# Kernel tuning notes

Hardware: AMD Instinct MI355X
Metric: run time of the kernel (lower is better)

Reference implementation:

```python
import jax, jax.numpy as jnp
import numpy as np

N, F_IN, HID, C, H = 4096, 1024, 64, 40, 8
ALPHA = 0.2  # LeakyReLU negative slope
NEG_INF = -9e15

def setup_inputs() -> dict:
    key = jax.random.key(0)
    ks = jax.random.split(key, 8)
    x = jax.random.normal(ks[0], (N, F_IN), jnp.float32)
    adj = jax.random.randint(ks[1], (N, N), 0, 2, jnp.int32)  # dense 0/1 adjacency
    W = jax.random.normal(ks[2], (H, F_IN, HID), jnp.float32) / np.sqrt(F_IN).astype(np.float32)
    a_src = jax.random.normal(ks[3], (H, HID), jnp.float32) * 0.1
    a_dst = jax.random.normal(ks[4], (H, HID), jnp.float32) * 0.1
    W_out = jax.random.normal(ks[5], (H * HID, C), jnp.float32) / np.sqrt(H * HID).astype(np.float32)
    ao_src = jax.random.normal(ks[6], (C,), jnp.float32) * 0.1
    ao_dst = jax.random.normal(ks[7], (C,), jnp.float32) * 0.1
    return dict(x=x, adj=adj, W=W, a_src=a_src, a_dst=a_dst,
                W_out=W_out, ao_src=ao_src, ao_dst=ao_dst)

def _masked_attention(src, dst, mask):
    # src: [..., N] scores for row node i; dst: [..., N] scores for col node j
    e = jax.nn.leaky_relu(src[..., :, None] + dst[..., None, :], ALPHA)  # [..., N, N]
    e = jnp.where(mask, e, NEG_INF)
    return jax.nn.softmax(e, axis=-1)

def reference(x, adj, W, a_src, a_dst, W_out, ao_src, ao_dst):
    mask = adj > 0  # [N, N]
    # multi-head GAT layer (concat=True)
    Wh = jnp.einsum('nf,hfo->hno', x, W)            # [H, N, HID]
    src = jnp.einsum('hno,ho->hn', Wh, a_src)       # [H, N]
    dst = jnp.einsum('hno,ho->hn', Wh, a_dst)       # [H, N]
    att = _masked_attention(src, dst, mask[None])   # [H, N, N]
    h = jnp.einsum('hij,hjo->hio', att, Wh)         # [H, N, HID]
    h = jax.nn.elu(h)                               # concat=True -> elu inside layer
    h = jnp.transpose(h, (1, 0, 2)).reshape(N, H * HID)  # concat heads -> [N, H*HID]
    # output GAT layer (concat=False -> no elu inside)
    Wh2 = h @ W_out                                 # [N, C]
    att2 = _masked_attention(Wh2 @ ao_src, Wh2 @ ao_dst, mask)  # [N, N]
    out = att2 @ Wh2                                # [N, C]
    # model-level: elu then log_softmax over classes
    return jax.nn.log_softmax(jax.nn.elu(out), axis=1)
```

## Files before the change

kernel.cpp:

```cpp
#include <hip/hip_runtime.h>

#define NN 4096
#define F_IN 1024
#define NHEAD 8
#define HID 64
#define NCLS 40
#define LOG2E 1.44269504f

typedef float f32x4 __attribute__((ext_vector_type(4)));
typedef float f32x2 __attribute__((ext_vector_type(2)));
typedef short s16x8 __attribute__((ext_vector_type(8)));

#define SWZ(r,c) (((r)*64) + ((c) ^ (((r)&7)<<3)))

__device__ __forceinline__ unsigned short f2bf(float f){
  unsigned u = __float_as_uint(f);
  return (unsigned short)((u + 0x7fffu + ((u >> 16) & 1u)) >> 16);
}
__device__ __forceinline__ float bf2f(unsigned short u){
  return __uint_as_float((unsigned)u << 16);
}
__device__ __forceinline__ unsigned cvtpk(float lo, float hi){
  unsigned r; asm("v_cvt_pk_bf16_f32 %0, %1, %2" : "=v"(r) : "v"(lo), "v"(hi)); return r;
}
__device__ __forceinline__ f32x2 pkmul(f32x2 a, f32x2 b){
  f32x2 r; asm("v_pk_mul_f32 %0, %1, %2" : "=v"(r) : "v"(a), "v"(b)); return r;
}

__global__ __launch_bounds__(256) void pack_adj_k(const int* __restrict__ adj, unsigned* __restrict__ bmT){
  int gid = blockIdx.x*256 + threadIdx.x;
  int lane = threadIdx.x & 63;
  unsigned long long m = __ballot(adj[gid] > 0);
  int w = gid >> 5, i = w >> 7, jw = w & 127;
  if (lane == 0)       bmT[(size_t)jw*NN + i] = (unsigned)m;
  else if (lane == 32) bmT[(size_t)jw*NN + i] = (unsigned)(m >> 32);
}

__global__ __launch_bounds__(256) void cast_W_k(const float* __restrict__ W, unsigned short* __restrict__ WbT){
  __shared__ float T[64][65];
  const int h = blockIdx.y, k0 = blockIdx.x*64, t = threadIdx.x;
  for (int idx = t; idx < 1024; idx += 256){
    int k = idx >> 4, c4 = idx & 15;
    *(float4*)&T[k][c4*4] = *(const float4*)&W[((size_t)h*F_IN + k0 + k)*HID + c4*4];
  }
  __syncthreads();
  for (int idx = t; idx < 512; idx += 256){
    int o = idx >> 3, ch = idx & 7;
    s16x8 v;
    #pragma unroll
    for (int e = 0; e < 8; ++e) v[e] = (short)f2bf(T[ch*8 + e][o]);
    *(s16x8*)&WbT[((size_t)h*HID + o)*F_IN + k0 + ch*8] = v;
  }
}

__global__ __launch_bounds__(256) void cast_Wo_k(const float* __restrict__ Wout, unsigned short* __restrict__ WoT){
  int idx = blockIdx.x*256 + threadIdx.x;
  int cc = idx >> 9, k = idx & 511;
  WoT[idx] = (cc < NCLS) ? f2bf(Wout[(size_t)k*NCLS + cc]) : (unsigned short)0;
}

__global__ __launch_bounds__(256) void gemm1_k(const float* __restrict__ x,
    const unsigned short* __restrict__ WbT, unsigned short* __restrict__ WhT,
    const float* __restrict__ a_src, const float* __restrict__ a_dst,
    float* __restrict__ srcv, float* __restrict__ dstv, float2* __restrict__ bdv){
  __shared__ unsigned short xS[64*64];
  __shared__ unsigned short wS[64*64];
  const int t = threadIdx.x, l = t & 63, wv = t >> 6, g = l >> 4, c = l & 15;
  const int h = blockIdx.y, n0 = blockIdx.x * 64;
  f32x4 acc[4] = {};
  for (int k0 = 0; k0 < F_IN; k0 += 64){
    __syncthreads();
    #pragma unroll
    for (int p = 0; p < 4; ++p){
      int idx = t + p*256, row = idx >> 4, c4 = idx & 15;
      float4 v = *(const float4*)&x[(size_t)(n0+row)*F_IN + k0 + c4*4];
      *(uint2*)&xS[SWZ(row, c4*4)] = make_uint2(cvtpk(v.x, v.y), cvtpk(v.z, v.w));
    }
    #pragma unroll
    for (int p = 0; p < 2; ++p){
      int idx = t + p*256, o = idx >> 3, ch = idx & 7;
      *(s16x8*)&wS[SWZ(o, ch*8)] = *(const s16x8*)&WbT[(size_t)(h*HID + o)*F_IN + k0 + ch*8];
    }
    __syncthreads();
    #pragma unroll
    for (int ks = 0; ks < 2; ++ks){
      s16x8 av = *(const s16x8*)&xS[SWZ(wv*16 + c, ks*32 + g*8)];
      #pragma unroll
      for (int ct = 0; ct < 4; ++ct){
        s16x8 bv = *(const s16x8*)&wS[SWZ(ct*16 + c, ks*32 + g*8)];
        acc[ct] = __builtin_amdgcn_mfma_f32_16x16x32_bf16(av, bv, acc[ct], 0, 0, 0);
      }
    }
  }
  float asv[4], adv[4];
  #pragma unroll
  for (int ct = 0; ct < 4; ++ct){ asv[ct] = a_src[h*HID + ct*16 + c]; adv[ct] = a_dst[h*HID + ct*16 + c]; }
  #pragma unroll
  for (int r = 0; r < 4; ++r){
    float ps = acc[0][r]*asv[0] + acc[1][r]*asv[1] + acc[2][r]*asv[2] + acc[3][r]*asv[3];
    float pd = acc[0][r]*adv[0] + acc[1][r]*adv[1] + acc[2][r]*adv[2] + acc[3][r]*adv[3];
    #pragma unroll
    for (int off = 1; off < 16; off <<= 1){ ps += __shfl_xor(ps, off); pd += __shfl_xor(pd, off); }
    if (c == 0){
      int n = n0 + wv*16 + g*4 + r;
      srcv[h*NN + n] = ps; dstv[h*NN + n] = pd;
      bdv[h*NN + n] = make_float2(exp2f(pd*LOG2E), exp2f(0.2f*pd*LOG2E));
    }
  }
  __syncthreads();
  #pragma unroll
  for (int ct = 0; ct < 4; ++ct)
    *(uint2*)&xS[SWZ(ct*16 + c, wv*16 + g*4)] = make_uint2(cvtpk(acc[ct][0], acc[ct][1]), cvtpk(acc[ct][2], acc[ct][3]));
  __syncthreads();
  #pragma unroll
  for (int p = 0; p < 2; ++p){
    int idx = t + p*256, o = idx >> 3, ch = idx & 7;
    *(s16x8*)&WhT[(size_t)(h*HID + o)*NN + n0 + ch*8] = *(const s16x8*)&xS[SWZ(o, ch*8)];
  }
}

__global__ __launch_bounds__(256) void maxred_k(const float* __restrict__ in, float* __restrict__ out){
  __shared__ float red[4];
  const float* p = in + (size_t)blockIdx.x*NN;
  float m = -3.0e38f;
  for (int i = threadIdx.x; i < NN; i += 256) m = fmaxf(m, p[i]);
  #pragma unroll
  for (int off = 32; off; off >>= 1) m = fmaxf(m, __shfl_xor(m, off));
  if ((threadIdx.x & 63) == 0) red[threadIdx.x >> 6] = m;
  __syncthreads();
  if (threadIdx.x == 0) out[blockIdx.x] = fmaxf(fmaxf(red[0], red[1]), fmaxf(red[2], red[3]));
}

template<int NCT, int NJT, int MODE>
__global__ __launch_bounds__(256) void agg_mfma_k(
    const unsigned* __restrict__ bmT, const unsigned short* __restrict__ VT,
    const float* __restrict__ srcv, const float2* __restrict__ bdv,
    const float* __restrict__ maxp, void* __restrict__ partOut, float* __restrict__ denOut)
{
  __shared__ unsigned short vS[2][NCT*16*64];
  __shared__ float2 dS[2][64];
  __shared__ unsigned bitS[2][2][64];
  const int t = threadIdx.x, l = t & 63, wv = t >> 6, g = l >> 4, c = l & 15;
  const int h  = (MODE == 0) ? (blockIdx.y >> 2) : 0;
  const int ck = (MODE == 0) ? (blockIdx.y & 3)  : blockIdx.y;
  const int jt0 = ck * NJT;
  const int i0 = blockIdx.x * 64;
  const int lr = wv*16 + c;
  const float sr = srcv[h*NN + i0 + lr];
  const float mx = maxp[MODE == 0 ? h : 0];
  const float tm = sr + mx;
  const float mi2 = fmaxf(tm, 0.2f*tm) * LOG2E;
  f32x2 ac2;
  ac2[0] = exp2f(fmaf(sr, LOG2E, -mi2));
  ac2[1] = exp2f(fmaf(0.2f*sr, LOG2E, -mi2));
  const unsigned short* vb = VT + (MODE == 0 ? (size_t)h*HID*NN : (size_t)0);
  const float2* bp = bdv + (MODE == 0 ? (size_t)h*NN : (size_t)0);

  f32x4 acc[NCT] = {};
  f32x4 accs = {};
  s16x8 ones;
  #pragma unroll
  for (int e = 0; e < 8; ++e) ones[e] = (short)0x3F80;

  s16x8 vreg[2]; float2 dreg = make_float2(0.f, 0.f); unsigned breg = 0;
  auto loadRegs = [&](int jt){
    #pragma unroll
    for (int p = 0; p < 2; ++p){
      int u = t + p*256;
      if (u < NCT*128){
        int o = u >> 3, chk = u & 7;
        vreg[p] = *(const s16x8*)&vb[(size_t)o*NN + jt*64 + chk*8];
      }
    }
    if (t < 64) { f32x2 bd = *(const f32x2*)&bp[jt*64 + t]; dreg = make_float2(bd[0], bd[1]); }
    else if (t < 192){ int u = t - 64; breg = bmT[(size_t)(jt*2 + (u>>6))*NN + i0 + (u & 63)]; }
  };
  auto writeLDS = [&](int b){
    #pragma unroll
    for (int p = 0; p < 2; ++p){
      int u = t + p*256;
      if (u < NCT*128){
        int o = u >> 3, chk = u & 7;
        *(s16x8*)&vS[b][SWZ(o, chk*8)] = vreg[p];
      }
    }
    if (t < 64) dS[b][t] = dreg;
    else if (t < 192){ int u = t - 64; bitS[b][u>>6][u&63] = breg; }
  };
  auto computeBuf = [&](int b){
    #pragma unroll
    for (int ks = 0; ks < 2; ++ks){
      unsigned wb = (bitS[b][ks][lr] >> (g*8)) & 0xffu;
      const f32x2* dr = (const f32x2*)&dS[b][ks*32 + g*8];
      float q[8];
      #pragma unroll
      for (int e = 0; e < 8; ++e){
        f32x2 pr = pkmul(ac2, dr[e]);
        float m3 = __builtin_amdgcn_fmed3f(pr[0], pr[1], 1.0f);
        q[e] = (wb & (1u << e)) ? m3 : 0.f;
      }
      s16x8 afr;
      ((unsigned*)&afr)[0] = cvtpk(q[0], q[1]);
      ((unsigned*)&afr)[1] = cvtpk(q[2], q[3]);
      ((unsigned*)&afr)[2] = cvtpk(q[4], q[5]);
      ((unsigned*)&afr)[3] = cvtpk(q[6], q[7]);
      #pragma unroll
      for (int ct = 0; ct < NCT; ++ct){
        s16x8 bv = *(const s16x8*)&vS[b][SWZ(ct*16 + c, ks*32 + g*8)];
        acc[ct] = __builtin_amdgcn_mfma_f32_16x16x32_bf16(afr, bv, acc[ct], 0, 0, 0);
      }
      accs = __builtin_amdgcn_mfma_f32_16x16x32_bf16(afr, ones, accs, 0, 0, 0);
    }
  };

  loadRegs(jt0);
  writeLDS(0);
  __syncthreads();
  int cur = 0;
  for (int jj = 0; jj < NJT; ++jj){
    const bool more = (jj + 1 < NJT);
    if (more) loadRegs(jt0 + jj + 1);
    computeBuf(cur);
    if (more) writeLDS(cur ^ 1);
    __syncthreads();
    cur ^= 1;
  }

  if (MODE == 0){
    unsigned short* ob = (unsigned short*)partOut + (size_t)ck * NN * (NHEAD*HID);
    #pragma unroll
    for (int r = 0; r < 4; ++r){
      int row = i0 + wv*16 + g*4 + r;
      #pragma unroll
      for (int ct = 0; ct < NCT; ++ct)
        ob[(size_t)row*(NHEAD*HID) + h*HID + ct*16 + c] = f2bf(acc[ct][r]);
      if (c == 0) denOut[(size_t)(ck*NHEAD + h)*NN + row] = accs[r];
    }
  } else {
    float* ob = (float*)partOut + (size_t)ck * NN * 64;
    #pragma unroll
    for (int r = 0; r < 4; ++r){
      int row = i0 + wv*16 + g*4 + r;
      #pragma unroll
      for (int ct = 0; ct < NCT; ++ct)
        ob[(size_t)row*64 + ct*16 + c] = acc[ct][r];
      if (c == 0) ob[(size_t)row*64 + 48] = accs[r];
    }
  }
}

__global__ __launch_bounds__(256) void merge1_k(const unsigned short* __restrict__ part,
                                                const float* __restrict__ den,
                                                unsigned short* __restrict__ hb){
  int idx = blockIdx.x*256 + threadIdx.x;
  int row = idx >> 7, q = idx & 127;
  int h = q >> 4;
  float v[4] = {0.f, 0.f, 0.f, 0.f};
  float dn = 0.f;
  #pragma unroll
  for (int ck = 0; ck < 4; ++ck){
    const unsigned short* pb = part + ((size_t)ck*NN + row)*(NHEAD*HID) + q*4;
    ushort4 u = *(const ushort4*)pb;
    v[0] += bf2f(u.x); v[1] += bf2f(u.y); v[2] += bf2f(u.z); v[3] += bf2f(u.w);
    dn += den[(size_t)(ck*NHEAD + h)*NN + row];
  }
  float inv = 1.f / fmaxf(dn, 1e-30f);
  #pragma unroll
  for (int e = 0; e < 4; ++e){
    float x = v[e]*inv;
    v[e] = x > 0.f ? x : __expf(x) - 1.f;
  }
  *(uint2*)&hb[(size_t)row*(NHEAD*HID) + q*4] = make_uint2(cvtpk(v[0], v[1]), cvtpk(v[2], v[3]));
}

__global__ __launch_bounds__(256) void gemm2_k(const unsigned short* __restrict__ hb,
    const unsigned short* __restrict__ WoT, const float* __restrict__ aos, const float* __restrict__ aod,
    unsigned short* __restrict__ WhT2, float* __restrict__ s2, float* __restrict__ d2,
    float2* __restrict__ bd2){
  __shared__ unsigned short aS[64*64];
  __shared__ unsigned short bS[48*64];
  const int t = threadIdx.x, l = t & 63, wv = t >> 6, g = l >> 4, c = l & 15;
  const int n0 = blockIdx.x * 64;
  f32x4 acc[3] = {};
  for (int k0 = 0; k0 < NHEAD*HID; k0 += 64){
    __syncthreads();
    #pragma unroll
    for (int p = 0; p < 2; ++p){
      int u = t + p*256, o = u >> 3, ch = u & 7;
      *(s16x8*)&aS[SWZ(o, ch*8)] = *(const s16x8*)&hb[(size_t)(n0+o)*(NHEAD*HID) + k0 + ch*8];
    }
    for (int u = t; u < 384; u += 256){
      int o = u >> 3, ch = u & 7;
      *(s16x8*)&bS[SWZ(o, ch*8)] = *(const s16x8*)&WoT[(size_t)o*(NHEAD*HID) + k0 + ch*8];
    }
    __syncthreads();
    #pragma unroll
    for (int ks = 0; ks < 2; ++ks){
      s16x8 av = *(const s16x8*)&aS[SWZ(wv*16 + c, ks*32 + g*8)];
      #pragma unroll
      for (int ct = 0; ct < 3; ++ct){
        s16x8 bv = *(const s16x8*)&bS[SWZ(ct*16 + c, ks*32 + g*8)];
        acc[ct] = __builtin_amdgcn_mfma_f32_16x16x32_bf16(av, bv, acc[ct], 0, 0, 0);
      }
    }
  }
  float asv[3], adv[3];
  #pragma unroll
  for (int ct = 0; ct < 3; ++ct){
    int col = ct*16 + c;
    asv[ct] = (col < NCLS) ? aos[col] : 0.f;
    adv[ct] = (col < NCLS) ? aod[col] : 0.f;
  }
  #pragma unroll
  for (int r = 0; r < 4; ++r){
    float ps = acc[0][r]*asv[0] + acc[1][r]*asv[1] + acc[2][r]*asv[2];
    float pd = acc[0][r]*adv[0] + acc[1][r]*adv[1] + acc[2][r]*adv[2];
    #pragma unroll
    for (int off = 1; off < 16; off <<= 1){ ps += __shfl_xor(ps, off); pd += __shfl_xor(pd, off); }
    if (c == 0){
      int n = n0 + wv*16 + g*4 + r;
      s2[n] = ps; d2[n] = pd;
      bd2[n] = make_float2(exp2f(pd*LOG2E), exp2f(0.2f*pd*LOG2E));
    }
  }
  __syncthreads();
  #pragma unroll
  for (int ct = 0; ct < 3; ++ct)
    *(uint2*)&bS[SWZ(ct*16 + c, wv*16 + g*4)] = make_uint2(cvtpk(acc[ct][0], acc[ct][1]), cvtpk(acc[ct][2], acc[ct][3]));
  __syncthreads();
  for (int u = t; u < 384; u += 256){
    int o = u >> 3, ch = u & 7;
    *(s16x8*)&WhT2[(size_t)o*NN + n0 + ch*8] = *(const s16x8*)&bS[SWZ(o, ch*8)];
  }
}

__global__ __launch_bounds__(256) void final_k(const float* __restrict__ part, float* __restrict__ out){
  const int wid = (blockIdx.x*256 + threadIdx.x) >> 6;
  const int c = threadIdx.x & 63;
  float acc = 0.f, rs = 0.f;
  #pragma unroll
  for (int ch = 0; ch < 16; ++ch){
    const float* pb = part + ((size_t)ch*NN + wid)*64;
    if (c < 48) acc += pb[c];
    rs += pb[48];
  }
  float v = acc / fmaxf(rs, 1e-30f);
  float e = v > 0.f ? v : __expf(v) - 1.f;
  float ev = (c < NCLS) ? e : -3.0e38f;
  float m = ev;
  #pragma unroll
  for (int off = 32; off; off >>= 1) m = fmaxf(m, __shfl_xor(m, off));
  float ex = (c < NCLS) ? __expf(e - m) : 0.f;
  float s = ex;
  #pragma unroll
  for (int off = 32; off; off >>= 1) s += __shfl_xor(s, off);
  if (c < NCLS) out[(size_t)wid*NCLS + c] = e - m - __logf(s);
}

extern "C" void kernel_launch(void* const* d_in, const int* in_sizes, int n_in,
                              void* d_out, int out_size, void* d_ws, size_t ws_size,
                              hipStream_t stream){
  (void)in_sizes; (void)n_in; (void)out_size; (void)ws_size;
  const float* x     = (const float*)d_in[0];
  const int*   adj   = (const int*)  d_in[1];
  const float* W     = (const float*)d_in[2];
  const float* a_src = (const float*)d_in[3];
  const float* a_dst = (const float*)d_in[4];
  const float* W_out = (const float*)d_in[5];
  const float* aos   = (const float*)d_in[6];
  const float* aod   = (const float*)d_in[7];
  float* out = (float*)d_out;

  char* p = (char*)d_ws;
  unsigned* bmT        = (unsigned*)p;       p += (size_t)NN*128*4;
  unsigned short* WbT  = (unsigned short*)p; p += (size_t)NHEAD*HID*F_IN*2;
  unsigned short* WhT  = (unsigned short*)p; p += (size_t)NHEAD*HID*NN*2;
  unsigned short* hbuf = (unsigned short*)p; p += (size_t)NN*NHEAD*HID*2;
  unsigned short* WoT  = (unsigned short*)p; p += (size_t)48*NHEAD*HID*2;
  unsigned short* WhT2 = (unsigned short*)p; p += (size_t)48*NN*2;
  float* srcv = (float*)p; p += (size_t)NHEAD*NN*4;
  float* dstv = (float*)p; p += (size_t)NHEAD*NN*4;
  float* maxd = (float*)p; p += 256;
  float* s2   = (float*)p; p += (size_t)NN*4;
  float* d2   = (float*)p; p += (size_t)NN*4;
  float* m2   = (float*)p; p += 256;
  float2* bdv1 = (float2*)p; p += (size_t)NHEAD*NN*8;
  float2* bdv2 = (float2*)p; p += (size_t)NN*8;
  float* den1 = (float*)p; p += (size_t)4*NHEAD*NN*4;
  char* partU = p; p += (size_t)16*NN*64*4;

  pack_adj_k<<<(NN*NN)/256, 256, 0, stream>>>(adj, bmT);
  cast_W_k<<<dim3(F_IN/64, NHEAD), 256, 0, stream>>>(W, WbT);
  cast_Wo_k<<<96, 256, 0, stream>>>(W_out, WoT);
  gemm1_k<<<dim3(NN/64, NHEAD), 256, 0, stream>>>(x, WbT, WhT, a_src, a_dst, srcv, dstv, bdv1);
  maxred_k<<<NHEAD, 256, 0, stream>>>(dstv, maxd);
  agg_mfma_k<4, 16, 0><<<dim3(NN/64, NHEAD*4), 256, 0, stream>>>(bmT, WhT, srcv, bdv1, maxd, partU, den1);
  merge1_k<<<(NN*128)/256, 256, 0, stream>>>((const unsigned short*)partU, den1, hbuf);
  gemm2_k<<<NN/64, 256, 0, stream>>>(hbuf, WoT, aos, aod, WhT2, s2, d2, bdv2);
  maxred_k<<<1, 256, 0, stream>>>(d2, m2);
  agg_mfma_k<3, 4, 1><<<dim3(NN/64, 16), 256, 0, stream>>>(bmT, WhT2, s2, bdv2, m2, partU, nullptr);
  final_k<<<NN/4, 256, 0, stream>>>((const float*)partU, out);
}
```

Before: 160.4 us.

## Use 32x32 MFMA tiles for layer-1 attention aggregation with 8-way j split

Replaces the layer-1 aggregation kernel with a dedicated version using 32x32x16 bf16 MFMA over 128-row tiles, covering all 64 hidden columns per wave. The denominator is now summed in VALU from the probabilities rather than by an extra MFMA against a ones vector. The j range is split into 8 chunks instead of 4, and the merge kernel and workspace sizes are updated to match. This aims to raise MFMA efficiency and reuse of the value tile per row block, at the cost of more partial outputs to write and merge.

Result: no change. 159.1 us (-0.8%).

```diff
diff --git a/kernel.cpp b/kernel.cpp
--- a/kernel.cpp
+++ b/kernel.cpp
@@ -9,6 +9,7 @@
 
 typedef float f32x4 __attribute__((ext_vector_type(4)));
 typedef float f32x2 __attribute__((ext_vector_type(2)));
+typedef float f32x16 __attribute__((ext_vector_type(16)));
 typedef short s16x8 __attribute__((ext_vector_type(8)));
 
 #define SWZ(r,c) (((r)*64) + ((c) ^ (((r)&7)<<3)))
@@ -131,67 +132,59 @@
   if (threadIdx.x == 0) out[blockIdx.x] = fmaxf(fmaxf(red[0], red[1]), fmaxf(red[2], red[3]));
 }
 
-template<int NCT, int NJT, int MODE>
-__global__ __launch_bounds__(256) void agg_mfma_k(
+template<int NJT>
+__global__ __launch_bounds__(256) void agg32_k(
     const unsigned* __restrict__ bmT, const unsigned short* __restrict__ VT,
     const float* __restrict__ srcv, const float2* __restrict__ bdv,
-    const float* __restrict__ maxp, void* __restrict__ partOut, float* __restrict__ denOut)
+    const float* __restrict__ maxp, unsigned short* __restrict__ partOut, float* __restrict__ denOut)
 {
-  __shared__ unsigned short vS[2][NCT*16*64];
+  __shared__ unsigned short vS[2][64*64];
   __shared__ float2 dS[2][64];
-  __shared__ unsigned bitS[2][2][64];
-  const int t = threadIdx.x, l = t & 63, wv = t >> 6, g = l >> 4, c = l & 15;
-  const int h  = (MODE == 0) ? (blockIdx.y >> 2) : 0;
-  const int ck = (MODE == 0) ? (blockIdx.y & 3)  : blockIdx.y;
+  __shared__ unsigned bitS[2][2][128];
+  const int t = threadIdx.x, l = t & 63, wv = t >> 6, hk = l >> 5, lr31 = l & 31;
+  const int h  = blockIdx.y >> 3;
+  const int ck = blockIdx.y & 7;
   const int jt0 = ck * NJT;
-  const int i0 = blockIdx.x * 64;
-  const int lr = wv*16 + c;
+  const int i0 = blockIdx.x * 128;
+  const int lr = wv*32 + lr31;
   const float sr = srcv[h*NN + i0 + lr];
-  const float mx = maxp[MODE == 0 ? h : 0];
+  const float mx = maxp[h];
   const float tm = sr + mx;
   const float mi2 = fmaxf(tm, 0.2f*tm) * LOG2E;
   f32x2 ac2;
   ac2[0] = exp2f(fmaf(sr, LOG2E, -mi2));
   ac2[1] = exp2f(fmaf(0.2f*sr, LOG2E, -mi2));
-  const unsigned short* vb = VT + (MODE == 0 ? (size_t)h*HID*NN : (size_t)0);
-  const float2* bp = bdv + (MODE == 0 ? (size_t)h*NN : (size_t)0);
-
-  f32x4 acc[NCT] = {};
-  f32x4 accs = {};
-  s16x8 ones;
-  #pragma unroll
-  for (int e = 0; e < 8; ++e) ones[e] = (short)0x3F80;
+  const unsigned short* vb = VT + (size_t)h*HID*NN;
+  const float2* bp = bdv + (size_t)h*NN;
+
+  f32x16 acc[2] = {};
+  float rs = 0.f;
 
   s16x8 vreg[2]; float2 dreg = make_float2(0.f, 0.f); unsigned breg = 0;
   auto loadRegs = [&](int jt){
     #pragma unroll
     for (int p = 0; p < 2; ++p){
-      int u = t + p*256;
-      if (u < NCT*128){
-        int o = u >> 3, chk = u & 7;
-        vreg[p] = *(const s16x8*)&vb[(size_t)o*NN + jt*64 + chk*8];
-      }
-    }
-    if (t < 64) { f32x2 bd = *(const f32x2*)&bp[jt*64 + t]; dreg = make_float2(bd[0], bd[1]); }
-    else if (t < 192){ int u = t - 64; breg = bmT[(size_t)(jt*2 + (u>>6))*NN + i0 + (u & 63)]; }
+      int u = t + p*256, o = u >> 3, chk = u & 7;
+      vreg[p] = *(const s16x8*)&vb[(size_t)o*NN + jt*64 + chk*8];
+    }
+    if (t < 64){ f32x2 bd = *(const f32x2*)&bp[jt*64 + t]; dreg = make_float2(bd[0], bd[1]); }
+    breg = bmT[(size_t)(jt*2 + (t>>7))*NN + i0 + (t & 127)];
   };
   auto writeLDS = [&](int b){
     #pragma unroll
     for (int p = 0; p < 2; ++p){
-      int u = t + p*256;
-      if (u < NCT*128){
-        int o = u >> 3, chk = u & 7;
-        *(s16x8*)&vS[b][SWZ(o, chk*8)] = vreg[p];
-      }
+      int u = t + p*256, o = u >> 3, chk = u & 7;
+      *(s16x8*)&vS[b][SWZ(o, chk*8)] = vreg[p];
     }
     if (t < 64) dS[b][t] = dreg;
-    else if (t < 192){ int u = t - 64; bitS[b][u>>6][u&63] = breg; }
+    bitS[b][t>>7][t & 127] = breg;
   };
   auto computeBuf = [&](int b){
     #pragma unroll
-    for (int ks = 0; ks < 2; ++ks){
-      unsigned wb = (bitS[b][ks][lr] >> (g*8)) & 0xffu;
-      const f32x2* dr = (const f32x2*)&dS[b][ks*32 + g*8];
+    for (int ksl = 0; ksl < 4; ++ksl){
+      const int b0 = ksl*16 + hk*8;
+      unsigned wb = (bitS[b][b0 >> 5][lr] >> (b0 & 31)) & 0xffu;
+      const f32x2* dr = (const f32x2*)&dS[b][b0];
       float q[8];
       #pragma unroll
       for (int e = 0; e < 8; ++e){
@@ -199,17 +192,17 @@
         float m3 = __builtin_amdgcn_fmed3f(pr[0], pr[1], 1.0f);
         q[e] = (wb & (1u << e)) ? m3 : 0.f;
       }
+      rs += ((q[0]+q[1])+(q[2]+q[3])) + ((q[4]+q[5])+(q[6]+q[7]));
       s16x8 afr;
       ((unsigned*)&afr)[0] = cvtpk(q[0], q[1]);
       ((unsigned*)&afr)[1] = cvtpk(q[2], q[3]);
       ((unsigned*)&afr)[2] = cvtpk(q[4], q[5]);
       ((unsigned*)&afr)[3] = cvtpk(q[6], q[7]);
       #pragma unroll
-      for (int ct = 0; ct < NCT; ++ct){
-        s16x8 bv = *(const s16x8*)&vS[b][SWZ(ct*16 + c, ks*32 + g*8)];
-        acc[ct] = __builtin_amdgcn_mfma_f32_16x16x32_bf16(afr, bv, acc[ct], 0, 0, 0);
-      }
-      accs = __builtin_amdgcn_mfma_f32_16x16x32_bf16(afr, ones, accs, 0, 0, 0);
+      for (int cf = 0; cf < 2; ++cf){
+        s16x8 bv = *(const s16x8*)&vS[b][SWZ(cf*32 + lr31, b0)];
+        acc[cf] = __builtin_amdgcn_mfma_f32_32x32x16_bf16(afr, bv, acc[cf], 0, 0, 0);
+      }
     }
   };
 
@@ -226,26 +219,123 @@
     cur ^= 1;
   }
 
-  if (MODE == 0){
-    unsigned short* ob = (unsigned short*)partOut + (size_t)ck * NN * (NHEAD*HID);
-    #pragma unroll
-    for (int r = 0; r < 4; ++r){
-      int row = i0 + wv*16 + g*4 + r;
-      #pragma unroll
-      for (int ct = 0; ct < NCT; ++ct)
-        ob[(size_t)row*(NHEAD*HID) + h*HID + ct*16 + c] = f2bf(acc[ct][r]);
-      if (c == 0) denOut[(size_t)(ck*NHEAD + h)*NN + row] = accs[r];
-    }
-  } else {
-    float* ob = (float*)partOut + (size_t)ck * NN * 64;
-    #pragma unroll
-    for (int r = 0; r < 4; ++r){
-      int row = i0 + wv*16 + g*4 + r;
-      #pragma unroll
-      for (int ct = 0; ct < NCT; ++ct)
-        ob[(size_t)row*64 + ct*16 + c] = acc[ct][r];
-      if (c == 0) ob[(size_t)row*64 + 48] = accs[r];
-    }
+  rs += __shfl_xor(rs, 32);
+  if (l < 32 && wv >= 0){
+    denOut[(size_t)(ck*NHEAD + h)*NN + i0 + wv*32 + l] = rs;
+  }
+  unsigned short* ob = partOut + (size_t)ck * NN * (NHEAD*HID);
+  #pragma unroll
+  for (int cf = 0; cf < 2; ++cf){
+    #pragma unroll
+    for (int r = 0; r < 16; ++r){
+      int row = i0 + wv*32 + (r & 3) + 8*(r >> 2) + 4*hk;
+      ob[(size_t)row*(NHEAD*HID) + h*HID + cf*32 + lr31] = f2bf(acc[cf][r]);
+    }
+  }
+}
+
+template<int NCT, int NJT>
+__global__ __launch_bounds__(256) void agg_mfma_k(
+    const unsigned* __restrict__ bmT, const unsigned short* __restrict__ VT,
+    const float* __restrict__ srcv, const float2* __restrict__ bdv,
+    const float* __restrict__ maxp, void* __restrict__ partOut)
+{
+  __shared__ unsigned short vS[2][NCT*16*64];
+  __shared__ float2 dS[2][64];
+  __shared__ unsigned bitS[2][2][64];
+  const int t = threadIdx.x, l = t & 63, wv = t >> 6, g = l >> 4, c = l & 15;
+  const int ck = blockIdx.y;
+  const int jt0 = ck * NJT;
+  const int i0 = blockIdx.x * 64;
+  const int lr = wv*16 + c;
+  const float sr = srcv[i0 + lr];
+  const float mx = maxp[0];
+  const float tm = sr + mx;
+  const float mi2 = fmaxf(tm, 0.2f*tm) * LOG2E;
+  f32x2 ac2;
+  ac2[0] = exp2f(fmaf(sr, LOG2E, -mi2));
+  ac2[1] = exp2f(fmaf(0.2f*sr, LOG2E, -mi2));
+  const unsigned short* vb = VT;
+  const float2* bp = bdv;
+
+  f32x4 acc[NCT] = {};
+  f32x4 accs = {};
+  s16x8 ones;
+  #pragma unroll
+  for (int e = 0; e < 8; ++e) ones[e] = (short)0x3F80;
+
+  s16x8 vreg[2]; float2 dreg = make_float2(0.f, 0.f); unsigned breg = 0;
+  auto loadRegs = [&](int jt){
+    #pragma unroll
+    for (int p = 0; p < 2; ++p){
+      int u = t + p*256;
+      if (u < NCT*128){
+        int o = u >> 3, chk = u & 7;
+        vreg[p] = *(const s16x8*)&vb[(size_t)o*NN + jt*64 + chk*8];
+      }
+    }
+    if (t < 64) { f32x2 bd = *(const f32x2*)&bp[jt*64 + t]; dreg = make_float2(bd[0], bd[1]); }
+    else if (t < 192){ int u = t - 64; breg = bmT[(size_t)(jt*2 + (u>>6))*NN + i0 + (u & 63)]; }
+  };
+  auto writeLDS = [&](int b){
+    #pragma unroll
+    for (int p = 0; p < 2; ++p){
+      int u = t + p*256;
+      if (u < NCT*128){
+        int o = u >> 3, chk = u & 7;
+        *(s16x8*)&vS[b][SWZ(o, chk*8)] = vreg[p];
+      }
+    }
+    if (t < 64) dS[b][t] = dreg;
+    else if (t < 192){ int u = t - 64; bitS[b][u>>6][u&63] = breg; }
+  };
+  auto computeBuf = [&](int b){
+    #pragma unroll
+    for (int ks = 0; ks < 2; ++ks){
+      unsigned wb = (bitS[b][ks][lr] >> (g*8)) & 0xffu;
+      const f32x2* dr = (const f32x2*)&dS[b][ks*32 + g*8];
+      float q[8];
+      #pragma unroll
+      for (int e = 0; e < 8; ++e){
+        f32x2 pr = pkmul(ac2, dr[e]);
+        float m3 = __builtin_amdgcn_fmed3f(pr[0], pr[1], 1.0f);
+        q[e] = (wb & (1u << e)) ? m3 : 0.f;
+      }
+      s16x8 afr;
+      ((unsigned*)&afr)[0] = cvtpk(q[0], q[1]);
+      ((unsigned*)&afr)[1] = cvtpk(q[2], q[3]);
+      ((unsigned*)&afr)[2] = cvtpk(q[4], q[5]);
+      ((unsigned*)&afr)[3] = cvtpk(q[6], q[7]);
+      #pragma unroll
+      for (int ct = 0; ct < NCT; ++ct){
+        s16x8 bv = *(const s16x8*)&vS[b][SWZ(ct*16 + c, ks*32 + g*8)];
+        acc[ct] = __builtin_amdgcn_mfma_f32_16x16x32_bf16(afr, bv, acc[ct], 0, 0, 0);
+      }
+      accs = __builtin_amdgcn_mfma_f32_16x16x32_bf16(afr, ones, accs, 0, 0, 0);
+    }
+  };
+
+  loadRegs(jt0);
+  writeLDS(0);
+  __syncthreads();
+  int cur = 0;
+  for (int jj = 0; jj < NJT; ++jj){
+    const bool more = (jj + 1 < NJT);
+    if (more) loadRegs(jt0 + jj + 1);
+    computeBuf(cur);
+    if (more) writeLDS(cur ^ 1);
+    __syncthreads();
+    cur ^= 1;
+  }
+
+  float* ob = (float*)partOut + (size_t)ck * NN * 64;
+  #pragma unroll
+  for (int r = 0; r < 4; ++r){
+    int row = i0 + wv*16 + g*4 + r;
+    #pragma unroll
+    for (int ct = 0; ct < NCT; ++ct)
+      ob[(size_t)row*64 + ct*16 + c] = acc[ct][r];
+    if (c == 0) ob[(size_t)row*64 + 48] = accs[r];
   }
 }
 
@@ -258,7 +348,7 @@
   float v[4] = {0.f, 0.f, 0.f, 0.f};
   float dn = 0.f;
   #pragma unroll
-  for (int ck = 0; ck < 4; ++ck){
+  for (int ck = 0; ck < 8; ++ck){
     const unsigned short* pb = part + ((size_t)ck*NN + row)*(NHEAD*HID) + q*4;
     ushort4 u = *(const ushort4*)pb;
     v[0] += bf2f(u.x); v[1] += bf2f(u.y); v[2] += bf2f(u.z); v[3] += bf2f(u.w);
@@ -386,18 +476,19 @@
   float* m2   = (float*)p; p += 256;
   float2* bdv1 = (float2*)p; p += (size_t)NHEAD*NN*8;
   float2* bdv2 = (float2*)p; p += (size_t)NN*8;
-  float* den1 = (float*)p; p += (size_t)4*NHEAD*NN*4;
-  char* partU = p; p += (size_t)16*NN*64*4;
+  float* den1 = (float*)p; p += (size_t)8*NHEAD*NN*4;
+  char* partU = p; p += (size_t)8*NN*512*2;
 
   pack_adj_k<<<(NN*NN)/256, 256, 0, stream>>>(adj, bmT);
   cast_W_k<<<dim3(F_IN/64, NHEAD), 256, 0, stream>>>(W, WbT);
   cast_Wo_k<<<96, 256, 0, stream>>>(W_out, WoT);
   gemm1_k<<<dim3(NN/64, NHEAD), 256, 0, stream>>>(x, WbT, WhT, a_src, a_dst, srcv, dstv, bdv1);
   maxred_k<<<NHEAD, 256, 0, stream>>>(dstv, maxd);
-  agg_mfma_k<4, 16, 0><<<dim3(NN/64, NHEAD*4), 256, 0, stream>>>(bmT, WhT, srcv, bdv1, maxd, partU, den1);
+  agg32_k<8><<<dim3(NN/128, NHEAD*8), 256, 0, stream>>>(bmT, WhT, srcv, bdv1, maxd,
+                                                        (unsigned short*)partU, den1);
   merge1_k<<<(NN*128)/256, 256, 0, stream>>>((const unsigned short*)partU, den1, hbuf);
   gemm2_k<<<NN/64, 256, 0, stream>>>(hbuf, WoT, aos, aod, WhT2, s2, d2, bdv2);
   maxred_k<<<1, 256, 0, stream>>>(d2, m2);
-  agg_mfma_k<3, 4, 1><<<dim3(NN/64, 16), 256, 0, stream>>>(bmT, WhT2, s2, bdv2, m2, partU, nullptr);
+  agg_mfma_k<3, 4><<<dim3(NN/64, 16), 256, 0, stream>>>(bmT, WhT2, s2, bdv2, m2, partU);
   final_k<<<NN/4, 256, 0, stream>>>((const float*)partU, out);
 }
```
